# Performance work log

Measured on AMD Instinct MI355X. Metric: run time of the kernel, lower is better.

## Reference

```python
import jax, jax.numpy as jnp
import numpy as np

V, S, B, E, H = 32000, 64, 64, 32, 16


def setup_inputs() -> dict:
    key = jax.random.key(0)
    k0, k1, k2, k3, k4, k5 = jax.random.split(key, 6)
    input_batch = jax.random.randint(k0, (S, B), 0, V)
    lookup = jax.random.uniform(k1, (V, E), dtype=jnp.float32)  # uniform_() in [0,1)
    bx = 1.0 / np.sqrt(E).astype(np.float32)
    bh = 1.0 / np.sqrt(H).astype(np.float32)
    weight_x = jax.random.uniform(k2, (E, H), minval=-bx, maxval=bx, dtype=jnp.float32)
    weight_h = jax.random.uniform(k3, (H, H), minval=-bh, maxval=bh, dtype=jnp.float32)
    weight_o = jax.random.uniform(k4, (H, V), minval=-bh, maxval=bh, dtype=jnp.float32)
    h0 = jax.random.uniform(k5, (H,), dtype=jnp.float32)  # initial hidden (torch code: random, never updated)
    return {"input_batch": input_batch, "lookup": lookup, "weight_x": weight_x,
            "weight_h": weight_h, "weight_o": weight_o, "h0": h0}


def reference(input_batch, lookup, weight_x, weight_h, weight_o, h0):
    # Embed: [S,B,E]
    X = lookup[input_batch]
    # NOTE: the original torch loop never reassigns H, so every timestep uses the
    # same initial hidden state -> the 'recurrence' contribution is a constant [H] vector.
    h_rec = h0 @ weight_h  # [H]
    H_table = jax.nn.sigmoid(jnp.einsum('sbe,eh->sbh', X, weight_x) + h_rec)  # [S,B,16]
    logits = jnp.einsum('sbh,hv->sbv', H_table, weight_o)  # [S,B,V]
    # original computes log(exp(x)/sum(exp(x))); stable equivalent:
    return jax.nn.log_softmax(logits, axis=-1)
```

## Files before the change

### kernel.cpp

```cpp
#include <hip/hip_runtime.h>
#include <hip/hip_bf16.h>

#define V_SIZE 32000
#define SEQ 64
#define BATCH 64
#define EMB 32
#define HID 16
#define NROWS (SEQ * BATCH)
#define V4 (V_SIZE / 4)
#define STRIPS 32
#define CHUNKS 64
#define ROWS_W (NROWS / CHUNKS)
#define RGROUP 8
#define NRB (NROWS / 16)
#define NTILES (V_SIZE / 16)
#define RBW 4
#define NRG (NRB / RBW)
#define XSTRIPS 100
#define TPW (NTILES / XSTRIPS)
#define NSLOTS XSTRIPS

typedef float f32x4 __attribute__((ext_vector_type(4)));
typedef short short8 __attribute__((ext_vector_type(8)));

__device__ inline short bf16_rne(float x) {
    unsigned u = __builtin_bit_cast(unsigned, x);
    unsigned r = u + 0x7FFFu + ((u >> 16) & 1u);
    return (short)(r >> 16);
}

__global__ __launch_bounds__(256) void k_htable(
    const int* __restrict__ idx, const float* __restrict__ lookup,
    const float* __restrict__ wx, const float* __restrict__ wh,
    const float* __restrict__ h0, float* __restrict__ h_table,
    short* __restrict__ a_frag)
{
    int r = blockIdx.x * 256 + threadIdx.x;
    if (r >= NROWS) return;

    float acc[HID];
    #pragma unroll
    for (int j = 0; j < HID; ++j) acc[j] = 0.f;

    #pragma unroll
    for (int i = 0; i < HID; ++i) {
        float h0i = h0[i];
        #pragma unroll
        for (int j = 0; j < HID; ++j) acc[j] += h0i * wh[i * HID + j];
    }

    int tok = idx[r];
    const float* xrow = lookup + (long)tok * EMB;
    #pragma unroll
    for (int e = 0; e < EMB; ++e) {
        float x = xrow[e];
        #pragma unroll
        for (int j = 0; j < HID; ++j) acc[j] += x * wx[e * HID + j];
    }

    float h[HID];
    #pragma unroll
    for (int j = 0; j < HID; ++j) {
        h[j] = 1.f / (1.f + __expf(-acc[j]));
        h_table[r * HID + j] = h[j];
    }

    const int rb = r >> 4;
    const int m  = r & 15;
    short8 lo, hi, zz;
    #pragma unroll
    for (int j = 0; j < 8; ++j) {
        lo[j] = bf16_rne(h[j]);
        hi[j] = bf16_rne(h[j + 8]);
        zz[j] = 0;
    }
    short8* af = reinterpret_cast<short8*>(a_frag);
    af[rb * 64 + m]      = lo;
    af[rb * 64 + m + 16] = hi;
    af[rb * 64 + m + 32] = zz;
    af[rb * 64 + m + 48] = zz;
}

__global__ __launch_bounds__(256) void k_wpack(
    const float* __restrict__ wo, short* __restrict__ b_frag)
{
    int gid = blockIdx.x * 256 + threadIdx.x;
    if (gid >= NTILES * 64) return;
    const int t = gid >> 6;
    const int l = gid & 63;
    const int col = t * 16 + (l & 15);

    short8 b;
    if (l < 32) {
        const int k0 = (l >> 4) * 8;
        #pragma unroll
        for (int j = 0; j < 8; ++j)
            b[j] = bf16_rne(wo[(size_t)(k0 + j) * V_SIZE + col]);
    } else {
        #pragma unroll
        for (int j = 0; j < 8; ++j) b[j] = 0;
    }
    reinterpret_cast<short8*>(b_frag)[gid] = b;
}

__global__ __launch_bounds__(256) void k_expsum(
    const short* __restrict__ a_frag, const short* __restrict__ b_frag,
    float* __restrict__ partial)
{
    const int lane = threadIdx.x & 63;
    const int wid  = threadIdx.x >> 6;
    const int g = blockIdx.x * 4 + wid;
    const int rbg = g & (NRG - 1);
    const int strip = g >> 6;

    const short8* af = reinterpret_cast<const short8*>(a_frag);
    const short8* bf = reinterpret_cast<const short8*>(b_frag);

    short8 a[RBW];
    #pragma unroll
    for (int i = 0; i < RBW; ++i)
        a[i] = af[(rbg * RBW + i) * 64 + lane];

    f32x4 acc[RBW];
    #pragma unroll
    for (int i = 0; i < RBW; ++i) acc[i] = (f32x4){0.f, 0.f, 0.f, 0.f};
    const f32x4 czero = {0.f, 0.f, 0.f, 0.f};

    const int t0 = strip * TPW;
    short8 bcur = bf[t0 * 64 + lane];
    short8 bnxt = bf[(t0 + 1) * 64 + lane];

    #pragma unroll 2
    for (int i = 0; i < TPW; ++i) {
        const int tp = t0 + i + 2;
        short8 bpre = bf[(tp < NTILES ? tp : NTILES - 1) * 64 + lane];

        f32x4 d[RBW];
        #pragma unroll
        for (int k = 0; k < RBW; ++k)
            d[k] = __builtin_amdgcn_mfma_f32_16x16x32_bf16(a[k], bcur, czero, 0, 0, 0);

        #pragma unroll
        for (int k = 0; k < RBW; ++k) {
            acc[k].x += __expf(d[k].x);
            acc[k].y += __expf(d[k].y);
            acc[k].z += __expf(d[k].z);
            acc[k].w += __expf(d[k].w);
        }

        bcur = bnxt;
        bnxt = bpre;
    }

    #pragma unroll
    for (int off = 1; off <= 8; off <<= 1) {
        #pragma unroll
        for (int k = 0; k < RBW; ++k) {
            acc[k].x += __shfl_xor(acc[k].x, off, 64);
            acc[k].y += __shfl_xor(acc[k].y, off, 64);
            acc[k].z += __shfl_xor(acc[k].z, off, 64);
            acc[k].w += __shfl_xor(acc[k].w, off, 64);
        }
    }

    if ((lane & 15) == 0) {
        #pragma unroll
        for (int k = 0; k < RBW; ++k) {
            const int rbase = (rbg * RBW + k) * 16 + (lane >> 4) * 4;
            float* p = partial + (size_t)strip * NROWS + rbase;
            p[0] = acc[k].x;
            p[1] = acc[k].y;
            p[2] = acc[k].z;
            p[3] = acc[k].w;
        }
    }
}

__global__ __launch_bounds__(256) void k_reduce(
    const float* __restrict__ partial, float* __restrict__ lse)
{
    int r = blockIdx.x * 256 + threadIdx.x;
    if (r >= NROWS) return;
    float s = 0.f;
    #pragma unroll
    for (int k = 0; k < NSLOTS; ++k)
        s += partial[(size_t)k * NROWS + r];
    lse[r] = __logf(s);
}

__global__ __launch_bounds__(256) void k_write(
    const float* __restrict__ h_table, const float* __restrict__ wo,
    const float* __restrict__ lse, float* __restrict__ out)
{
    const int tid = threadIdx.x;
    const int strip = blockIdx.x & (STRIPS - 1);
    const int chunk = blockIdx.x / STRIPS;
    const int v4 = strip * 256 + tid;
    const bool act = v4 < V4;
    const int r0 = chunk * ROWS_W;

    const f32x4* wo4 = reinterpret_cast<const f32x4*>(wo);
    f32x4 w[HID];
    #pragma unroll
    for (int j = 0; j < HID; ++j) {
        if (act) w[j] = wo4[j * V4 + v4];
        else     w[j] = (f32x4){0.f, 0.f, 0.f, 0.f};
    }

    f32x4* out4 = reinterpret_cast<f32x4*>(out);

    for (int rr = r0; rr < r0 + ROWS_W; rr += RGROUP) {
        f32x4 acc[RGROUP];
        #pragma unroll
        for (int i = 0; i < RGROUP; ++i) acc[i] = (f32x4){0.f, 0.f, 0.f, 0.f};

        #pragma unroll
        for (int q = 0; q < 4; ++q) {
            f32x4 h4[RGROUP];
            #pragma unroll
            for (int i = 0; i < RGROUP; ++i)
                h4[i] = *reinterpret_cast<const f32x4*>(h_table + (rr + i) * HID + q * 4);
            #pragma unroll
            for (int i = 0; i < RGROUP; ++i) {
                acc[i] += h4[i].x * w[q * 4 + 0];
                acc[i] += h4[i].y * w[q * 4 + 1];
                acc[i] += h4[i].z * w[q * 4 + 2];
                acc[i] += h4[i].w * w[q * 4 + 3];
            }
        }

        const f32x4 ls0 = *reinterpret_cast<const f32x4*>(lse + rr);
        const f32x4 ls1 = *reinterpret_cast<const f32x4*>(lse + rr + 4);

        if (act) {
            #pragma unroll
            for (int i = 0; i < RGROUP; ++i) {
                float l = (i < 4) ? ls0[i & 3] : ls1[i & 3];
                f32x4 o = acc[i] - l;
                out4[(long)(rr + i) * V4 + v4] = o;
            }
        }
    }
}

extern "C" void kernel_launch(void* const* d_in, const int* in_sizes, int n_in,
                              void* d_out, int out_size, void* d_ws, size_t ws_size,
                              hipStream_t stream) {
    const int*   idx    = (const int*)d_in[0];
    const float* lookup = (const float*)d_in[1];
    const float* wx     = (const float*)d_in[2];
    const float* wh     = (const float*)d_in[3];
    const float* wo     = (const float*)d_in[4];
    const float* h0     = (const float*)d_in[5];
    float* out = (float*)d_out;

    float* h_table = (float*)d_ws;
    float* lse     = h_table + NROWS * HID;
    float* partial = lse + NROWS;
    short* a_frag  = (short*)(partial + NSLOTS * NROWS);
    short* b_frag  = a_frag + NRB * 64 * 8;

    k_htable<<<NROWS / 256, 256, 0, stream>>>(idx, lookup, wx, wh, h0, h_table, a_frag);
    k_wpack<<<(NTILES * 64) / 256, 256, 0, stream>>>(wo, b_frag);
    k_expsum<<<(NRG * XSTRIPS) / 4, 256, 0, stream>>>(a_frag, b_frag, partial);
    k_reduce<<<NROWS / 256, 256, 0, stream>>>(partial, lse);
    k_write<<<STRIPS * CHUNKS, 256, 0, stream>>>(h_table, wo, lse, out);
}
```

Before: 187.2 us.

## Merge prep kernels, retile exp-sum and rotate B tile start per wave

Fuses the hidden-table and weight-pack kernels into one launch that branches on block index, removing a kernel launch. It changes exp-sum tiling from 4 row-blocks per wave over 100 vocab strips to 2 row-blocks over 50 strips. It also staggers each wave's starting tile within its strip by row-group index, so concurrent waves read different B fragments and contend less on the same cache lines. Fewer row-blocks per wave means B fragments are reused less across MFMAs, but each wave runs longer and needs fewer registers.

```diff
diff --git a/kernel.cpp b/kernel.cpp
--- a/kernel.cpp
+++ b/kernel.cpp
@@ -14,11 +14,13 @@
 #define RGROUP 8
 #define NRB (NROWS / 16)
 #define NTILES (V_SIZE / 16)
-#define RBW 4
+#define RBW 2
 #define NRG (NRB / RBW)
-#define XSTRIPS 100
+#define XSTRIPS 50
 #define TPW (NTILES / XSTRIPS)
 #define NSLOTS XSTRIPS
+#define HT_BLOCKS (NROWS / 256)
+#define WP_BLOCKS (NTILES * 64 / 256)
 
 typedef float f32x4 __attribute__((ext_vector_type(4)));
 typedef short short8 __attribute__((ext_vector_type(8)));
@@ -29,78 +31,75 @@
     return (short)(r >> 16);
 }
 
-__global__ __launch_bounds__(256) void k_htable(
+__global__ __launch_bounds__(256) void k_prep(
     const int* __restrict__ idx, const float* __restrict__ lookup,
     const float* __restrict__ wx, const float* __restrict__ wh,
-    const float* __restrict__ h0, float* __restrict__ h_table,
-    short* __restrict__ a_frag)
-{
-    int r = blockIdx.x * 256 + threadIdx.x;
-    if (r >= NROWS) return;
-
-    float acc[HID];
-    #pragma unroll
-    for (int j = 0; j < HID; ++j) acc[j] = 0.f;
-
-    #pragma unroll
-    for (int i = 0; i < HID; ++i) {
-        float h0i = h0[i];
-        #pragma unroll
-        for (int j = 0; j < HID; ++j) acc[j] += h0i * wh[i * HID + j];
-    }
-
-    int tok = idx[r];
-    const float* xrow = lookup + (long)tok * EMB;
-    #pragma unroll
-    for (int e = 0; e < EMB; ++e) {
-        float x = xrow[e];
-        #pragma unroll
-        for (int j = 0; j < HID; ++j) acc[j] += x * wx[e * HID + j];
-    }
-
-    float h[HID];
-    #pragma unroll
-    for (int j = 0; j < HID; ++j) {
-        h[j] = 1.f / (1.f + __expf(-acc[j]));
-        h_table[r * HID + j] = h[j];
-    }
-
-    const int rb = r >> 4;
-    const int m  = r & 15;
-    short8 lo, hi, zz;
-    #pragma unroll
-    for (int j = 0; j < 8; ++j) {
-        lo[j] = bf16_rne(h[j]);
-        hi[j] = bf16_rne(h[j + 8]);
-        zz[j] = 0;
-    }
-    short8* af = reinterpret_cast<short8*>(a_frag);
-    af[rb * 64 + m]      = lo;
-    af[rb * 64 + m + 16] = hi;
-    af[rb * 64 + m + 32] = zz;
-    af[rb * 64 + m + 48] = zz;
-}
-
-__global__ __launch_bounds__(256) void k_wpack(
-    const float* __restrict__ wo, short* __restrict__ b_frag)
-{
-    int gid = blockIdx.x * 256 + threadIdx.x;
-    if (gid >= NTILES * 64) return;
-    const int t = gid >> 6;
-    const int l = gid & 63;
-    const int col = t * 16 + (l & 15);
-
-    short8 b;
-    if (l < 32) {
-        const int k0 = (l >> 4) * 8;
-        #pragma unroll
-        for (int j = 0; j < 8; ++j)
-            b[j] = bf16_rne(wo[(size_t)(k0 + j) * V_SIZE + col]);
+    const float* __restrict__ h0, const float* __restrict__ wo,
+    float* __restrict__ h_table, short* __restrict__ a_frag,
+    short* __restrict__ b_frag)
+{
+    if (blockIdx.x < HT_BLOCKS) {
+        int r = blockIdx.x * 256 + threadIdx.x;
+
+        float acc[HID];
+        #pragma unroll
+        for (int j = 0; j < HID; ++j) acc[j] = 0.f;
+
+        #pragma unroll
+        for (int i = 0; i < HID; ++i) {
+            float h0i = h0[i];
+            #pragma unroll
+            for (int j = 0; j < HID; ++j) acc[j] += h0i * wh[i * HID + j];
+        }
+
+        int tok = idx[r];
+        const float* xrow = lookup + (long)tok * EMB;
+        #pragma unroll
+        for (int e = 0; e < EMB; ++e) {
+            float x = xrow[e];
+            #pragma unroll
+            for (int j = 0; j < HID; ++j) acc[j] += x * wx[e * HID + j];
+        }
+
+        float h[HID];
+        #pragma unroll
+        for (int j = 0; j < HID; ++j) {
+            h[j] = 1.f / (1.f + __expf(-acc[j]));
+            h_table[r * HID + j] = h[j];
+        }
+
+        const int rb = r >> 4;
+        const int m  = r & 15;
+        short8 lo, hi, zz;
+        #pragma unroll
+        for (int j = 0; j < 8; ++j) {
+            lo[j] = bf16_rne(h[j]);
+            hi[j] = bf16_rne(h[j + 8]);
+            zz[j] = 0;
+        }
+        short8* af = reinterpret_cast<short8*>(a_frag);
+        af[rb * 64 + m]      = lo;
+        af[rb * 64 + m + 16] = hi;
+        af[rb * 64 + m + 32] = zz;
+        af[rb * 64 + m + 48] = zz;
     } else {
-        #pragma unroll
-        for (int j = 0; j < 8; ++j) b[j] = 0;
-    }
-    reinterpret_cast<short8*>(b_frag)[gid] = b;
+        int gid = (blockIdx.x - HT_BLOCKS) * 256 + threadIdx.x;
+        const int t = gid >> 6;
+        const int l = gid & 63;
+        const int col = t * 16 + (l & 15);
+
+        short8 b;
+        if (l < 32) {
+            const int k0 = (l >> 4) * 8;
+            #pragma unroll
+            for (int j = 0; j < 8; ++j)
+                b[j] = bf16_rne(wo[(size_t)(k0 + j) * V_SIZE + col]);
+        } else {
+            #pragma unroll
+            for (int j = 0; j < 8; ++j) b[j] = 0;
+        }
+        reinterpret_cast<short8*>(b_frag)[gid] = b;
+    }
 }
 
 __global__ __launch_bounds__(256) void k_expsum(
@@ -111,7 +110,7 @@
     const int wid  = threadIdx.x >> 6;
     const int g = blockIdx.x * 4 + wid;
     const int rbg = g & (NRG - 1);
-    const int strip = g >> 6;
+    const int strip = g >> 7;
 
     const short8* af = reinterpret_cast<const short8*>(a_frag);
     const short8* bf = reinterpret_cast<const short8*>(b_frag);
@@ -121,19 +120,23 @@
     for (int i = 0; i < RBW; ++i)
         a[i] = af[(rbg * RBW + i) * 64 + lane];
 
+    const f32x4 czero = {0.f, 0.f, 0.f, 0.f};
+    const int t0 = strip * TPW;
+    const int tend = t0 + TPW;
+    const int rot = rbg % TPW;
+
     f32x4 acc[RBW];
     #pragma unroll
     for (int i = 0; i < RBW; ++i) acc[i] = (f32x4){0.f, 0.f, 0.f, 0.f};
-    const f32x4 czero = {0.f, 0.f, 0.f, 0.f};
-
-    const int t0 = strip * TPW;
-    short8 bcur = bf[t0 * 64 + lane];
-    short8 bnxt = bf[(t0 + 1) * 64 + lane];
-
-    #pragma unroll 2
+
+    int t  = t0 + rot;
+    int tn = t + 1;  if (tn == tend) tn = t0;
+    short8 bcur = bf[t * 64 + lane];
+    short8 bnxt = bf[tn * 64 + lane];
+
     for (int i = 0; i < TPW; ++i) {
-        const int tp = t0 + i + 2;
-        short8 bpre = bf[(tp < NTILES ? tp : NTILES - 1) * 64 + lane];
+        int tp = tn + 1;  if (tp == tend) tp = t0;
+        short8 bpre = bf[tp * 64 + lane];
 
         f32x4 d[RBW];
         #pragma unroll
@@ -150,6 +153,7 @@
 
         bcur = bnxt;
         bnxt = bpre;
+        tn = tp;
     }
 
     #pragma unroll
@@ -260,8 +264,8 @@
     short* a_frag  = (short*)(partial + NSLOTS * NROWS);
     short* b_frag  = a_frag + NRB * 64 * 8;
 
-    k_htable<<<NROWS / 256, 256, 0, stream>>>(idx, lookup, wx, wh, h0, h_table, a_frag);
-    k_wpack<<<(NTILES * 64) / 256, 256, 0, stream>>>(wo, b_frag);
+    k_prep<<<HT_BLOCKS + WP_BLOCKS, 256, 0, stream>>>(idx, lookup, wx, wh, h0, wo,
+                                                      h_table, a_frag, b_frag);
     k_expsum<<<(NRG * XSTRIPS) / 4, 256, 0, stream>>>(a_frag, b_frag, partial);
     k_reduce<<<NROWS / 256, 256, 0, stream>>>(partial, lse);
     k_write<<<STRIPS * CHUNKS, 256, 0, stream>>>(h_table, wo, lse, out);
```

Result: faster. 161.0 us (-14.0%).
